# Performance work log

Measured on AMD Instinct MI355X. Metric: run time of the kernel, lower is better.

## Reference

```python
import jax, jax.numpy as jnp
import numpy as np

B, N, D, H = 4, 512, 256, 256


def setup_inputs() -> dict:
    key = jax.random.key(0)
    ks = jax.random.split(key, 8)
    s = lambda fan: 1.0 / np.sqrt(fan)
    return {
        "X": jax.random.normal(ks[0], (B, N, D), dtype=jnp.float32),
        "Y": jax.random.normal(ks[1], (B, N, D), dtype=jnp.float32),
        # fc = Linear(D,H) -> Tanh -> Linear(H,H)
        "W1": jax.random.normal(ks[2], (H, D), dtype=jnp.float32) * s(D),
        "b1": jnp.zeros((H,), dtype=jnp.float32),
        "W2": jax.random.normal(ks[3], (H, H), dtype=jnp.float32) * s(H),
        "b2": jnp.zeros((H,), dtype=jnp.float32),
        # fc_q, fc_k
        "Wq": jax.random.normal(ks[4], (H, H), dtype=jnp.float32) * s(H),
        "bq": jnp.zeros((H,), dtype=jnp.float32),
        "Wk": jax.random.normal(ks[5], (H, H), dtype=jnp.float32) * s(H),
        "bk": jnp.zeros((H,), dtype=jnp.float32),
        # AddComp projection vector v: E_ij = v . tanh(Q_i + K_j)
        "v": jax.random.normal(ks[6], (H,), dtype=jnp.float32) * s(H),
        "k": 5,
    }


def reference(X, Y, W1, b1, W2, b2, Wq, bq, Wk, bk, v, k):
    # fc: Linear -> Tanh -> Linear  (Y and k are unused, as in the original)
    h = jnp.tanh(jnp.einsum('bnd,hd->bnh', X, W1) + b1)
    h = jnp.einsum('bnh,gh->bng', h, W2) + b2          # [B,N,H]
    Q = jnp.einsum('bnh,gh->bng', h, Wq) + bq          # [B,N,H]
    K = jnp.einsum('bnh,gh->bng', h, Wk) + bk          # [B,N,H]
    # Additive compatibility: E[b,i,j] = v . tanh(Q[b,i] + K[b,j])
    E = jnp.einsum('bijh,h->bij', jnp.tanh(Q[:, :, None, :] + K[:, None, :, :]), v)
    # Symmetrize
    return 0.5 * (E + jnp.swapaxes(E, -2, -1))
```

## Files before the change

### kernel.cpp

```cpp
#include <hip/hip_runtime.h>


typedef float f2 __attribute__((ext_vector_type(2)));
typedef float f4 __attribute__((ext_vector_type(4)));
typedef float f32x4 __attribute__((ext_vector_type(4)));
typedef __bf16 bf16x8 __attribute__((ext_vector_type(8)));

#define C2F 2.8853900817779268f

__device__ inline unsigned short f2bf(float f) {
    unsigned u = __float_as_uint(f);
    unsigned r = (u + 0x7fffu + ((u >> 16) & 1u)) >> 16;
    return (unsigned short)r;
}
__device__ inline float bf2f(unsigned short h) {
    return __uint_as_float(((unsigned)h) << 16);
}

__device__ inline void split4(const f4 a, unsigned short* hp, unsigned short* lp) {
    unsigned short h[4], l[4];
#pragma unroll
    for (int t = 0; t < 4; ++t) {
        h[t] = f2bf(a[t]);
        l[t] = f2bf(a[t] - bf2f(h[t]));
    }
    uint2 hv, lv;
    hv.x = (unsigned)h[0] | ((unsigned)h[1] << 16);
    hv.y = (unsigned)h[2] | ((unsigned)h[3] << 16);
    lv.x = (unsigned)l[0] | ((unsigned)l[1] << 16);
    lv.y = (unsigned)l[2] | ((unsigned)l[3] << 16);
    *(uint2*)hp = hv;
    *(uint2*)lp = lv;
}

template <int ACT>
__global__ __launch_bounds__(256) void gemm_fullk(
    const float* __restrict__ A, const float* __restrict__ Wa,
    const float* __restrict__ Wb, const float* __restrict__ ba,
    const float* __restrict__ bb2, float* __restrict__ C, int Nn) {
    __shared__ unsigned short sAhi[64][264];
    __shared__ unsigned short sAlo[64][264];
    __shared__ unsigned short sBhi[64][264];
    __shared__ unsigned short sBlo[64][264];

    const int tid = threadIdx.x;
    const int m0 = blockIdx.x << 6;
    const int n0 = blockIdx.y << 6;

    const float* Atile = A + (size_t)m0 * 256;
    const float* Wtile = (n0 < 256) ? (Wa + (size_t)n0 * 256)
                                    : (Wb + (size_t)(n0 - 256) * 256);
    const int col4 = (tid & 63) << 2;
    const int rgrp = tid >> 6;
#pragma unroll
    for (int t = 0; t < 16; ++t) {
        const int row = (t << 2) + rgrp;
        f4 av = *(const f4*)&Atile[(size_t)row * 256 + col4];
        f4 wv = *(const f4*)&Wtile[(size_t)row * 256 + col4];
        split4(av, &sAhi[row][col4], &sAlo[row][col4]);
        split4(wv, &sBhi[row][col4], &sBlo[row][col4]);
    }
    __syncthreads();

    const int lane = tid & 63;
    const int wav = tid >> 6;
    const int wm = wav >> 1, wn = wav & 1;
    const int fr = lane & 15;
    const int fks = (lane >> 4) << 3;

    f32x4 acc[2][2];
#pragma unroll
    for (int i = 0; i < 2; ++i)
#pragma unroll
        for (int j = 0; j < 2; ++j) acc[i][j] = (f32x4){0.f, 0.f, 0.f, 0.f};

#pragma unroll
    for (int kt = 0; kt < 256; kt += 32) {
        bf16x8 ah[2], al[2], bh[2], bl[2];
#pragma unroll
        for (int s = 0; s < 2; ++s) {
            ah[s] = *(const bf16x8*)&sAhi[(wm << 5) + (s << 4) + fr][kt + fks];
            al[s] = *(const bf16x8*)&sAlo[(wm << 5) + (s << 4) + fr][kt + fks];
            bh[s] = *(const bf16x8*)&sBhi[(wn << 5) + (s << 4) + fr][kt + fks];
            bl[s] = *(const bf16x8*)&sBlo[(wn << 5) + (s << 4) + fr][kt + fks];
        }
#pragma unroll
        for (int i = 0; i < 2; ++i)
#pragma unroll
            for (int j = 0; j < 2; ++j) {
                acc[i][j] = __builtin_amdgcn_mfma_f32_16x16x32_bf16(ah[i], bh[j], acc[i][j], 0, 0, 0);
                acc[i][j] = __builtin_amdgcn_mfma_f32_16x16x32_bf16(ah[i], bl[j], acc[i][j], 0, 0, 0);
                acc[i][j] = __builtin_amdgcn_mfma_f32_16x16x32_bf16(al[i], bh[j], acc[i][j], 0, 0, 0);
            }
    }

    const int rbase = (lane >> 4) << 2;
#pragma unroll
    for (int i = 0; i < 2; ++i) {
#pragma unroll
        for (int j = 0; j < 2; ++j) {
            const int gcol = n0 + (wn << 5) + (j << 4) + fr;
            const float bias = (ACT == 2 && gcol >= 256) ? bb2[gcol - 256] : ba[gcol];
#pragma unroll
            for (int q = 0; q < 4; ++q) {
                const int grow = m0 + (wm << 5) + (i << 4) + rbase + q;
                float x = acc[i][j][q] + bias;
                if (ACT == 1)
                    x = 1.0f - 2.0f * __builtin_amdgcn_rcpf(
                                          1.0f + __builtin_amdgcn_exp2f(C2F * x));
                if (ACT == 2)
                    x = fminf(__builtin_amdgcn_exp2f(C2F * x), 1.0e4f);
                C[(size_t)grow * Nn + gcol] = x;
            }
        }
    }
}

__global__ __launch_bounds__(256) void gemm_stage1(
    const float* __restrict__ X, const float* __restrict__ W1,
    const float* __restrict__ b1, const float* __restrict__ Wq,
    const float* __restrict__ Wk, const float* __restrict__ W2,
    const float* __restrict__ b2, const float* __restrict__ bq,
    const float* __restrict__ bk, float* __restrict__ h1,
    float* __restrict__ Wc, float* __restrict__ bc) {
    __shared__ unsigned short sAhi[64][264];
    __shared__ unsigned short sAlo[64][264];
    __shared__ unsigned short sBhi[64][264];
    __shared__ unsigned short sBlo[64][264];
    __shared__ float sred[64][4];

    const int tid = threadIdx.x;
    const bool is_nt = (blockIdx.x >= 128);
    const int blk = is_nt ? (blockIdx.x - 128) : blockIdx.x;
    const int m0 = (is_nt ? (blk >> 2) : (blk >> 2)) << 6;
    const int n0 = (blk & 3) << 6;

    const int col4 = (tid & 63) << 2;
    const int rgrp = tid >> 6;

    if (!is_nt) {
        const float* Atile = X + (size_t)m0 * 256;
        const float* Wtile = W1 + (size_t)n0 * 256;
#pragma unroll
        for (int t = 0; t < 16; ++t) {
            const int row = (t << 2) + rgrp;
            f4 av = *(const f4*)&Atile[(size_t)row * 256 + col4];
            f4 wv = *(const f4*)&Wtile[(size_t)row * 256 + col4];
            split4(av, &sAhi[row][col4], &sAlo[row][col4]);
            split4(wv, &sBhi[row][col4], &sBlo[row][col4]);
        }
    } else {
        const float* Atile = (m0 < 256) ? (Wq + (size_t)m0 * 256)
                                        : (Wk + (size_t)(m0 - 256) * 256);
#pragma unroll
        for (int t = 0; t < 16; ++t) {
            const int row = (t << 2) + rgrp;
            f4 av = *(const f4*)&Atile[(size_t)row * 256 + col4];
            split4(av, &sAhi[row][col4], &sAlo[row][col4]);
        }
        const int c4 = (tid & 15) << 2;
        const int kg = tid >> 4;
#pragma unroll
        for (int t = 0; t < 16; ++t) {
            const int k = (t << 4) + kg;
            f4 wv = *(const f4*)&W2[(size_t)k * 256 + n0 + c4];
#pragma unroll
            for (int q = 0; q < 4; ++q) {
                unsigned short hi = f2bf(wv[q]);
                sBhi[c4 + q][k] = hi;
                sBlo[c4 + q][k] = f2bf(wv[q] - bf2f(hi));
            }
        }
    }
    __syncthreads();

    const int lane = tid & 63;
    const int wav = tid >> 6;
    const int wm = wav >> 1, wn = wav & 1;
    const int fr = lane & 15;
    const int fks = (lane >> 4) << 3;

    f32x4 acc[2][2];
#pragma unroll
    for (int i = 0; i < 2; ++i)
#pragma unroll
        for (int j = 0; j < 2; ++j) acc[i][j] = (f32x4){0.f, 0.f, 0.f, 0.f};

#pragma unroll
    for (int kt = 0; kt < 256; kt += 32) {
        bf16x8 ah[2], al[2], bh[2], bl[2];
#pragma unroll
        for (int s = 0; s < 2; ++s) {
            ah[s] = *(const bf16x8*)&sAhi[(wm << 5) + (s << 4) + fr][kt + fks];
            al[s] = *(const bf16x8*)&sAlo[(wm << 5) + (s << 4) + fr][kt + fks];
            bh[s] = *(const bf16x8*)&sBhi[(wn << 5) + (s << 4) + fr][kt + fks];
            bl[s] = *(const bf16x8*)&sBlo[(wn << 5) + (s << 4) + fr][kt + fks];
        }
#pragma unroll
        for (int i = 0; i < 2; ++i)
#pragma unroll
            for (int j = 0; j < 2; ++j) {
                acc[i][j] = __builtin_amdgcn_mfma_f32_16x16x32_bf16(ah[i], bh[j], acc[i][j], 0, 0, 0);
                acc[i][j] = __builtin_amdgcn_mfma_f32_16x16x32_bf16(ah[i], bl[j], acc[i][j], 0, 0, 0);
                acc[i][j] = __builtin_amdgcn_mfma_f32_16x16x32_bf16(al[i], bh[j], acc[i][j], 0, 0, 0);
            }
    }

    const int rbase = (lane >> 4) << 2;
    if (!is_nt) {
#pragma unroll
        for (int i = 0; i < 2; ++i)
#pragma unroll
            for (int j = 0; j < 2; ++j) {
                const int gcol = n0 + (wn << 5) + (j << 4) + fr;
                const float bias = b1[gcol];
#pragma unroll
                for (int q = 0; q < 4; ++q) {
                    const int grow = m0 + (wm << 5) + (i << 4) + rbase + q;
                    float x = acc[i][j][q] + bias;
                    x = 1.0f - 2.0f * __builtin_amdgcn_rcpf(
                                          1.0f + __builtin_amdgcn_exp2f(C2F * x));
                    h1[(size_t)grow * 256 + gcol] = x;
                }
            }
    } else {
#pragma unroll
        for (int i = 0; i < 2; ++i)
#pragma unroll
            for (int j = 0; j < 2; ++j) {
                const int gcol = n0 + (wn << 5) + (j << 4) + fr;
#pragma unroll
                for (int q = 0; q < 4; ++q) {
                    const int grow = m0 + (wm << 5) + (i << 4) + rbase + q;
                    Wc[(size_t)grow * 256 + gcol] = acc[i][j][q];
                }
            }
        if ((blk & 3) == 0) {
            const int rr = tid >> 2;
            const int part = (tid & 3) << 6;
            const int grow = m0 + rr;
            const float* Ar = (grow < 256) ? &Wq[(size_t)grow * 256]
                                           : &Wk[(size_t)(grow - 256) * 256];
            float s = 0.f;
#pragma unroll
            for (int e = 0; e < 64; e += 4) {
                f4 a = *(const f4*)&Ar[part + e];
                f4 bv = *(const f4*)&b2[part + e];
                s += a[0] * bv[0] + a[1] * bv[1] + a[2] * bv[2] + a[3] * bv[3];
            }
            sred[rr][tid & 3] = s;
            __syncthreads();
            if (tid < 64) {
                float bias = sred[tid][0] + sred[tid][1] + sred[tid][2] + sred[tid][3];
                const int g2 = m0 + tid;
                bias += (g2 < 256) ? bq[g2] : bk[g2 - 256];
                bc[g2] = bias;
            }
        }
    }
}

__global__ __launch_bounds__(512, 4) void pairwise_kernel(
    const float* __restrict__ uwb, const float* __restrict__ v,
    float* __restrict__ Ep) {
    __shared__ float sU[2][64][68];
    __shared__ float sW[2][64][68];
    __shared__ float sV[128];

    const int tid = threadIdx.x;
    const int bb = blockIdx.x;
    const int hh = (bb & 1) << 7;
    const int tt = bb >> 1;
    const int b = tt >> 6;
    const int i0 = ((tt >> 3) & 7) << 6;
    const int j0 = (tt & 7) << 6;

    const float* ubase = uwb + (size_t)((b << 9) + i0) * 512 + hh;
    const float* wbase = uwb + (size_t)((b << 9) + j0) * 512 + 256 + hh;

    const int sr = tid >> 3;
    const int sc = (tid & 7) << 3;

    {
        f4 a0 = *(const f4*)&ubase[(size_t)sr * 512 + sc];
        f4 a1 = *(const f4*)&ubase[(size_t)sr * 512 + sc + 4];
        f4 b0 = *(const f4*)&wbase[(size_t)sr * 512 + sc];
        f4 b1 = *(const f4*)&wbase[(size_t)sr * 512 + sc + 4];
        *(f4*)&sU[0][sr][sc] = a0;
        *(f4*)&sU[0][sr][sc + 4] = a1;
        *(f4*)&sW[0][sr][sc] = b0;
        *(f4*)&sW[0][sr][sc + 4] = b1;
    }
    if (tid < 32) *(f4*)&sV[tid << 2] = *(const f4*)&v[hh + (tid << 2)];
    __syncthreads();

    const int ty = tid >> 5;
    const int tx = tid & 31;

    float acc[4][2];
#pragma unroll
    for (int d = 0; d < 4; ++d)
#pragma unroll
        for (int e = 0; e < 2; ++e) acc[d][e] = 0.f;

    const f2 one2 = (f2){1.f, 1.f};

#define COMPUTE_CHUNK(buf, vb)                                                 \
    {                                                                          \
        _Pragma("unroll 2") for (int h4 = 0; h4 < 64; h4 += 4) {               \
            f4 vv = *(const f4*)&sV[(vb) + h4];                                \
            f4 uu[4], ww[2];                                                   \
            _Pragma("unroll") for (int d = 0; d < 4; ++d)                      \
                uu[d] = *(const f4*)&sU[buf][ty + (d << 4)][h4];               \
            _Pragma("unroll") for (int e = 0; e < 2; ++e)                      \
                ww[e] = *(const f4*)&sW[buf][tx + (e << 5)][h4];               \
            _Pragma("unroll") for (int d = 0; d < 4; ++d)                      \
            _Pragma("unroll") for (int e = 0; e < 2; ++e) {                    \
                f2 u01 = (f2){uu[d][0], uu[d][1]};                             \
                f2 u23 = (f2){uu[d][2], uu[d][3]};                             \
                f2 w01 = (f2){ww[e][0], ww[e][1]};                             \
                f2 w23 = (f2){ww[e][2], ww[e][3]};                             \
                f2 A01 = __builtin_elementwise_fma(u01, w01, one2);            \
                f2 A23 = __builtin_elementwise_fma(u23, w23, one2);            \
                float m01 = A01.x * A01.y;                                     \
                float m23 = A23.x * A23.y;                                     \
                float P = m01 * m23;                                           \
                float t01 = fmaf(vv[0], A01.y, vv[1] * A01.x);                 \
                float t23 = fmaf(vv[2], A23.y, vv[3] * A23.x);                 \
                float Nm = fmaf(t01, m23, t23 * m01);                          \
                acc[d][e] = fmaf(Nm, __builtin_amdgcn_rcpf(P), acc[d][e]);     \
            }                                                                  \
        }                                                                      \
    }

    f4 pa0 = *(const f4*)&ubase[(size_t)sr * 512 + 64 + sc];
    f4 pa1 = *(const f4*)&ubase[(size_t)sr * 512 + 64 + sc + 4];
    f4 pb0 = *(const f4*)&wbase[(size_t)sr * 512 + 64 + sc];
    f4 pb1 = *(const f4*)&wbase[(size_t)sr * 512 + 64 + sc + 4];

    COMPUTE_CHUNK(0, 0)

    *(f4*)&sU[1][sr][sc] = pa0;
    *(f4*)&sU[1][sr][sc + 4] = pa1;
    *(f4*)&sW[1][sr][sc] = pb0;
    *(f4*)&sW[1][sr][sc + 4] = pb1;
    __syncthreads();

    COMPUTE_CHUNK(1, 64)
#undef COMPUTE_CHUNK

    float* ep = Ep + (size_t)(bb & 1) * 1048576 +
                (size_t)((b << 9) + i0) * 512 + j0;
#pragma unroll
    for (int d = 0; d < 4; ++d)
#pragma unroll
        for (int e = 0; e < 2; ++e)
            ep[(size_t)(ty + (d << 4)) * 512 + tx + (e << 5)] = acc[d][e];
}

__global__ __launch_bounds__(256) void sym_kernel(const float* __restrict__ Ep,
                                                  const float* __restrict__ v,
                                                  float* __restrict__ out) {
    __shared__ float t1[64][65];
    __shared__ float t2[64][65];
    __shared__ float red[4];

    const int tid = threadIdx.x;
    const int lane = tid & 63, wv = tid >> 6;

    float x = v[tid];
#pragma unroll
    for (int o = 32; o > 0; o >>= 1) x += __shfl_xor(x, o, 64);
    if (lane == 0) red[wv] = x;

    const int bb = blockIdx.x;
    const int b = bb >> 6;
    const int i0 = ((bb >> 3) & 7) << 6;
    const int j0 = (bb & 7) << 6;

    for (int idx = tid; idx < 4096; idx += 256) {
        const int r = idx >> 6, c = idx & 63;
        const size_t o1 = (size_t)((b << 9) + i0 + r) * 512 + j0 + c;
        const size_t o2 = (size_t)((b << 9) + j0 + r) * 512 + i0 + c;
        t1[r][c] = Ep[o1] + Ep[o1 + 1048576];
        t2[r][c] = Ep[o2] + Ep[o2 + 1048576];
    }
    __syncthreads();
    const float Sv = red[0] + red[1] + red[2] + red[3];
    for (int idx = tid; idx < 4096; idx += 256) {
        const int r = idx >> 6, c = idx & 63;
        out[(size_t)((b << 9) + i0 + r) * 512 + j0 + c] = Sv - (t1[r][c] + t2[c][r]);
    }
}

extern "C" void kernel_launch(void* const* d_in, const int* in_sizes, int n_in,
                              void* d_out, int out_size, void* d_ws, size_t ws_size,
                              hipStream_t stream) {
    const float* X  = (const float*)d_in[0];
    const float* W1 = (const float*)d_in[2];
    const float* b1 = (const float*)d_in[3];
    const float* W2 = (const float*)d_in[4];
    const float* b2 = (const float*)d_in[5];
    const float* Wq = (const float*)d_in[6];
    const float* bq = (const float*)d_in[7];
    const float* Wk = (const float*)d_in[8];
    const float* bk = (const float*)d_in[9];
    const float* v  = (const float*)d_in[10];

    float* ws  = (float*)d_ws;
    float* h1  = ws;
    float* uwb = ws + 524288;
    float* Wc  = ws + 1572864;
    float* bc  = ws + 1703936;
    float* Ep  = ws + 1704448;
    float* out = (float*)d_out;

    gemm_stage1<<<160, 256, 0, stream>>>(X, W1, b1, Wq, Wk, W2, b2, bq, bk,
                                         h1, Wc, bc);
    gemm_fullk<2><<<dim3(32, 8), 256, 0, stream>>>(h1, Wc, Wc + 65536, bc,
                                                   bc + 256, uwb, 512);
    pairwise_kernel<<<512, 512, 0, stream>>>(uwb, v, Ep);
    sym_kernel<<<256, 256, 0, stream>>>(Ep, v, out);
}
```

Measured before the change: 61.60 us.

## Split pairwise hidden dimension into four slices and simplify per-pair math

The pairwise kernel now splits the hidden dimension into four 64-wide slices instead of two 128-wide ones. This doubles the grid to 1024 blocks, removes the in-kernel double buffering and halves shared memory per block so the launch bound can allow 8 blocks. The rational tanh evaluation now uses one reciprocal per pair of hidden elements instead of one per four, trading a few more rcp instructions for fewer multiplies and better conditioning. The symmetrize kernel now sums four partial buffers, which doubles the Ep workspace traffic.

```diff
diff --git a/kernel.cpp b/kernel.cpp
--- a/kernel.cpp
+++ b/kernel.cpp
@@ -132,7 +132,7 @@
     const int tid = threadIdx.x;
     const bool is_nt = (blockIdx.x >= 128);
     const int blk = is_nt ? (blockIdx.x - 128) : blockIdx.x;
-    const int m0 = (is_nt ? (blk >> 2) : (blk >> 2)) << 6;
+    const int m0 = (blk >> 2) << 6;
     const int n0 = (blk & 3) << 6;
 
     const int col4 = (tid & 63) << 2;
@@ -260,38 +260,38 @@
     }
 }
 
-__global__ __launch_bounds__(512, 4) void pairwise_kernel(
+__global__ __launch_bounds__(512, 8) void pairwise_kernel(
     const float* __restrict__ uwb, const float* __restrict__ v,
     float* __restrict__ Ep) {
-    __shared__ float sU[2][64][68];
-    __shared__ float sW[2][64][68];
-    __shared__ float sV[128];
+    __shared__ float sU[64][68];
+    __shared__ float sW[64][68];
+    __shared__ float sV[64];
 
     const int tid = threadIdx.x;
     const int bb = blockIdx.x;
-    const int hh = (bb & 1) << 7;
-    const int tt = bb >> 1;
+    const int hcs = bb & 3;
+    const int hc = hcs << 6;
+    const int tt = bb >> 2;
     const int b = tt >> 6;
     const int i0 = ((tt >> 3) & 7) << 6;
     const int j0 = (tt & 7) << 6;
 
-    const float* ubase = uwb + (size_t)((b << 9) + i0) * 512 + hh;
-    const float* wbase = uwb + (size_t)((b << 9) + j0) * 512 + 256 + hh;
+    const float* ubase = uwb + (size_t)((b << 9) + i0) * 512 + hc;
+    const float* wbase = uwb + (size_t)((b << 9) + j0) * 512 + 256 + hc;
 
     const int sr = tid >> 3;
     const int sc = (tid & 7) << 3;
-
     {
         f4 a0 = *(const f4*)&ubase[(size_t)sr * 512 + sc];
         f4 a1 = *(const f4*)&ubase[(size_t)sr * 512 + sc + 4];
         f4 b0 = *(const f4*)&wbase[(size_t)sr * 512 + sc];
         f4 b1 = *(const f4*)&wbase[(size_t)sr * 512 + sc + 4];
-        *(f4*)&sU[0][sr][sc] = a0;
-        *(f4*)&sU[0][sr][sc + 4] = a1;
-        *(f4*)&sW[0][sr][sc] = b0;
-        *(f4*)&sW[0][sr][sc + 4] = b1;
-    }
-    if (tid < 32) *(f4*)&sV[tid << 2] = *(const f4*)&v[hh + (tid << 2)];
+        *(f4*)&sU[sr][sc] = a0;
+        *(f4*)&sU[sr][sc + 4] = a1;
+        *(f4*)&sW[sr][sc] = b0;
+        *(f4*)&sW[sr][sc + 4] = b1;
+    }
+    if (tid < 16) *(f4*)&sV[tid << 2] = *(const f4*)&v[hc + (tid << 2)];
     __syncthreads();
 
     const int ty = tid >> 5;
@@ -305,52 +305,34 @@
 
     const f2 one2 = (f2){1.f, 1.f};
 
-#define COMPUTE_CHUNK(buf, vb)                                                 \
-    {                                                                          \
-        _Pragma("unroll 2") for (int h4 = 0; h4 < 64; h4 += 4) {               \
-            f4 vv = *(const f4*)&sV[(vb) + h4];                                \
-            f4 uu[4], ww[2];                                                   \
-            _Pragma("unroll") for (int d = 0; d < 4; ++d)                      \
-                uu[d] = *(const f4*)&sU[buf][ty + (d << 4)][h4];               \
-            _Pragma("unroll") for (int e = 0; e < 2; ++e)                      \
-                ww[e] = *(const f4*)&sW[buf][tx + (e << 5)][h4];               \
-            _Pragma("unroll") for (int d = 0; d < 4; ++d)                      \
-            _Pragma("unroll") for (int e = 0; e < 2; ++e) {                    \
-                f2 u01 = (f2){uu[d][0], uu[d][1]};                             \
-                f2 u23 = (f2){uu[d][2], uu[d][3]};                             \
-                f2 w01 = (f2){ww[e][0], ww[e][1]};                             \
-                f2 w23 = (f2){ww[e][2], ww[e][3]};                             \
-                f2 A01 = __builtin_elementwise_fma(u01, w01, one2);            \
-                f2 A23 = __builtin_elementwise_fma(u23, w23, one2);            \
-                float m01 = A01.x * A01.y;                                     \
-                float m23 = A23.x * A23.y;                                     \
-                float P = m01 * m23;                                           \
-                float t01 = fmaf(vv[0], A01.y, vv[1] * A01.x);                 \
-                float t23 = fmaf(vv[2], A23.y, vv[3] * A23.x);                 \
-                float Nm = fmaf(t01, m23, t23 * m01);                          \
-                acc[d][e] = fmaf(Nm, __builtin_amdgcn_rcpf(P), acc[d][e]);     \
-            }                                                                  \
-        }                                                                      \
-    }
-
-    f4 pa0 = *(const f4*)&ubase[(size_t)sr * 512 + 64 + sc];
-    f4 pa1 = *(const f4*)&ubase[(size_t)sr * 512 + 64 + sc + 4];
-    f4 pb0 = *(const f4*)&wbase[(size_t)sr * 512 + 64 + sc];
-    f4 pb1 = *(const f4*)&wbase[(size_t)sr * 512 + 64 + sc + 4];
-
-    COMPUTE_CHUNK(0, 0)
-
-    *(f4*)&sU[1][sr][sc] = pa0;
-    *(f4*)&sU[1][sr][sc + 4] = pa1;
-    *(f4*)&sW[1][sr][sc] = pb0;
-    *(f4*)&sW[1][sr][sc + 4] = pb1;
-    __syncthreads();
-
-    COMPUTE_CHUNK(1, 64)
-#undef COMPUTE_CHUNK
-
-    float* ep = Ep + (size_t)(bb & 1) * 1048576 +
-                (size_t)((b << 9) + i0) * 512 + j0;
+#pragma unroll 4
+    for (int h4 = 0; h4 < 64; h4 += 4) {
+        f4 vv = *(const f4*)&sV[h4];
+        f4 uu[4], ww[2];
+#pragma unroll
+        for (int d = 0; d < 4; ++d) uu[d] = *(const f4*)&sU[ty + (d << 4)][h4];
+#pragma unroll
+        for (int e = 0; e < 2; ++e) ww[e] = *(const f4*)&sW[tx + (e << 5)][h4];
+#pragma unroll
+        for (int d = 0; d < 4; ++d)
+#pragma unroll
+            for (int e = 0; e < 2; ++e) {
+                f2 u01 = (f2){uu[d][0], uu[d][1]};
+                f2 u23 = (f2){uu[d][2], uu[d][3]};
+                f2 w01 = (f2){ww[e][0], ww[e][1]};
+                f2 w23 = (f2){ww[e][2], ww[e][3]};
+                f2 A01 = __builtin_elementwise_fma(u01, w01, one2);
+                f2 A23 = __builtin_elementwise_fma(u23, w23, one2);
+                float m01 = A01.x * A01.y;
+                float t01 = fmaf(vv[0], A01.y, vv[1] * A01.x);
+                acc[d][e] = fmaf(t01, __builtin_amdgcn_rcpf(m01), acc[d][e]);
+                float m23 = A23.x * A23.y;
+                float t23 = fmaf(vv[2], A23.y, vv[3] * A23.x);
+                acc[d][e] = fmaf(t23, __builtin_amdgcn_rcpf(m23), acc[d][e]);
+            }
+    }
+
+    float* ep = Ep + (size_t)hcs * 1048576 + (size_t)((b << 9) + i0) * 512 + j0;
 #pragma unroll
     for (int d = 0; d < 4; ++d)
 #pragma unroll
@@ -382,8 +364,10 @@
         const int r = idx >> 6, c = idx & 63;
         const size_t o1 = (size_t)((b << 9) + i0 + r) * 512 + j0 + c;
         const size_t o2 = (size_t)((b << 9) + j0 + r) * 512 + i0 + c;
-        t1[r][c] = Ep[o1] + Ep[o1 + 1048576];
-        t2[r][c] = Ep[o2] + Ep[o2 + 1048576];
+        t1[r][c] = (Ep[o1] + Ep[o1 + 1048576]) +
+                   (Ep[o1 + 2097152] + Ep[o1 + 3145728]);
+        t2[r][c] = (Ep[o2] + Ep[o2 + 1048576]) +
+                   (Ep[o2 + 2097152] + Ep[o2 + 3145728]);
     }
     __syncthreads();
     const float Sv = red[0] + red[1] + red[2] + red[3];
@@ -419,6 +403,6 @@
                                          h1, Wc, bc);
     gemm_fullk<2><<<dim3(32, 8), 256, 0, stream>>>(h1, Wc, Wc + 65536, bc,
                                                    bc + 256, uwb, 512);
-    pairwise_kernel<<<512, 512, 0, stream>>>(uwb, v, Ep);
+    pairwise_kernel<<<1024, 512, 0, stream>>>(uwb, v, Ep);
     sym_kernel<<<256, 256, 0, stream>>>(Ep, v, out);
 }
```

After: 81.88 us. +32.9%, slower.
